# Kernel tuning notes

Hardware: AMD Instinct MI355X
Metric: run time of the kernel (lower is better)

## Reference

```python
import jax, jax.numpy as jnp
import numpy as np

N_BATCH = 1024   # batch size (P=256 identities x K=4 instances)
M_PARTS = 8      # local stripes per image
D_FEAT = 128     # local feature dim
K_PER_ID = 4
MARGIN = 0.3
EPS = 1e-12


def setup_inputs() -> dict:
    key = jax.random.key(0)
    inputs = jax.random.normal(key, (N_BATCH, M_PARTS, D_FEAT), dtype=jnp.float32)
    labels = jnp.arange(N_BATCH, dtype=jnp.int64) // K_PER_ID  # equal samples per class
    return {"inputs": inputs, "labels": labels}


def _shortest_dist(dmat):
    """DTW-style monotone shortest path over the (m, n) grid.
    dmat: [m, n, N, N] -> returns [N, N].
    """
    m = dmat.shape[0]
    # first row: only moves to the right -> cumulative sum over j
    row = jnp.cumsum(dmat[0], axis=0)  # [n, N, N]
    inf = jnp.full(dmat.shape[2:], jnp.inf, dtype=dmat.dtype)

    def step(carry, inp):
        d_ij, up = inp                       # each [N, N]
        val = jnp.minimum(carry, up) + d_ij  # carry=inf at j=0 -> picks `up`
        return val, val

    for i in range(1, m):  # m is a small structural constant (stripes)
        _, row = jax.lax.scan(step, inf, (dmat[i], row))
    return row[-1]  # dist[m-1][n-1], shape [N, N]


def _local_dist(x):
    """x: [N, m, d] (already L2-normalized) -> pairwise aligned dist [N, N]."""
    N, m, d = x.shape
    xf = x.reshape(N * m, d)
    sq = jnp.sum(xf * xf, axis=1)
    dist = sq[:, None] + sq[None, :] - 2.0 * (xf @ xf.T)   # [Nm, Nm]
    dist = jnp.sqrt(jnp.clip(dist, EPS, None))
    dist = jnp.tanh(dist * 0.5)  # (e^d - 1) / (e^d + 1)
    dist = dist.reshape(N, m, N, m).transpose(1, 3, 0, 2)   # [m, n, N, N]
    return _shortest_dist(dist)


def reference(inputs, labels):
    # normalize local features to unit length
    x = inputs / (jnp.linalg.norm(inputs, axis=-1, keepdims=True) + EPS)
    dist_mat = _local_dist(x)  # [N, N]

    # hard example mining
    is_pos = labels[:, None] == labels[None, :]
    dist_ap = jnp.max(jnp.where(is_pos, dist_mat, -jnp.inf), axis=1)
    dist_an = jnp.min(jnp.where(is_pos, jnp.inf, dist_mat), axis=1)

    # MarginRankingLoss(margin)(dist_an, dist_ap, y=1)
    loss = jnp.mean(jnp.maximum(dist_ap - dist_an + MARGIN, 0.0))
    return loss
```

## Files before the change

kernel.cpp:

```cpp
#include <hip/hip_runtime.h>
#include <hip/hip_bf16.h>
#include <math.h>

#define NB 1024
#define MP 8
#define DF 128
#define NV (NB*MP)
#define EPSR 1e-12f
#define MARGIN_ 0.3f

#define GC0  0.4999965f
#define GC1 -0.0416276f
#define GC2  0.0040808f
#define GC3 -0.00035138f
#define GC4  0.00001765f

typedef __bf16    bf16x8 __attribute__((ext_vector_type(8)));
typedef float     f32x4  __attribute__((ext_vector_type(4)));
typedef _Float16  f16x4  __attribute__((ext_vector_type(4)));
typedef _Float16  f16x8  __attribute__((ext_vector_type(8)));

__global__ __launch_bounds__(256) void norm_kernel(const float* __restrict__ x,
                                                   unsigned short* __restrict__ xnb,
                                                   unsigned* __restrict__ ap_max,
                                                   unsigned* __restrict__ an_min) {
    if (blockIdx.x == 0) {
        for (int i = threadIdx.x; i < NB; i += 256) {
            ap_max[i] = 0u;
            an_min[i] = 0x7F800000u;
        }
    }
    const int wave = threadIdx.x >> 6;
    const int lane = threadIdx.x & 63;
    const int v = blockIdx.x * 4 + wave;
    const float e0 = x[v * DF + lane];
    const float e1 = x[v * DF + 64 + lane];
    float s = e0 * e0 + e1 * e1;
    #pragma unroll
    for (int off = 32; off > 0; off >>= 1) s += __shfl_xor(s, off);
    const float inv = 1.0f / (sqrtf(s) + EPSR);
    const __hip_bfloat16 b0 = __float2bfloat16(e0 * inv);
    const __hip_bfloat16 b1 = __float2bfloat16(e1 * inv);
    xnb[v * DF + lane]      = *(const unsigned short*)&b0;
    xnb[v * DF + 64 + lane] = *(const unsigned short*)&b1;
}

__global__ __launch_bounds__(256) void dist_kernel(const unsigned short* __restrict__ xnb,
                                                   const int* __restrict__ labels,
                                                   unsigned* __restrict__ ap_max,
                                                   unsigned* __restrict__ an_min) {
    __shared__ alignas(16) unsigned char smem[32768];
    unsigned short* As = (unsigned short*)smem;
    unsigned short* Bs = (unsigned short*)(smem + 16384);
    unsigned short* E  = (unsigned short*)smem;

    const int idx = (int)blockIdx.x;
    float fsq = sqrtf(8.0f * (float)idx + 1.0f);
    int by = (int)((fsq - 1.0f) * 0.5f);
    while ((by + 1) * (by + 2) / 2 <= idx) ++by;
    while (by * (by + 1) / 2 > idx) --by;
    const int bx = idx - by * (by + 1) / 2;

    const int t    = threadIdx.x;
    const int wave = t >> 6;
    const int lane = t & 63;
    const int wr   = wave >> 1;
    const int wc   = wave & 1;
    const int aBase = bx * 16;
    const int bBase = by * 16;

    const int fr = lane & 15;
    const int fq = lane >> 4;

    f32x4 acc[4][4];
    #pragma unroll
    for (int tr = 0; tr < 4; ++tr)
        #pragma unroll
        for (int tc = 0; tc < 4; ++tc) acc[tr][tc] = (f32x4){0.f, 0.f, 0.f, 0.f};

    #pragma unroll
    for (int kci = 0; kci < 2; ++kci) {
        const int kc = kci * 64;
        if (kci) __syncthreads();
        #pragma unroll
        for (int i = 0; i < 8; ++i) {
            const int ldi  = t + i * 256;
            const int side = ldi >> 10;
            const int r    = (ldi >> 3) & 127;
            const int ch   = ldi & 7;
            const int gv   = (side ? bBase : aBase) * MP + r;
            const uint4 v  = *(const uint4*)&xnb[gv * DF + kc + ch * 8];
            unsigned short* dst = side ? Bs : As;
            *(uint4*)&dst[r * 64 + ((ch ^ (r & 7)) * 8)] = v;
        }
        __syncthreads();

        #pragma unroll
        for (int ksl = 0; ksl < 2; ++ksl) {
            bf16x8 af[4], bfr[4];
            const int ch = ksl * 4 + fq;
            #pragma unroll
            for (int tr = 0; tr < 4; ++tr) {
                const int va = wr * 64 + tr * 16 + fr;
                af[tr] = *(const bf16x8*)&As[va * 64 + ((ch ^ (fr & 7)) * 8)];
            }
            #pragma unroll
            for (int tc = 0; tc < 4; ++tc) {
                const int vb = wc * 64 + tc * 16 + fr;
                bfr[tc] = *(const bf16x8*)&Bs[vb * 64 + ((ch ^ (fr & 7)) * 8)];
            }
            #pragma unroll
            for (int tr = 0; tr < 4; ++tr)
                #pragma unroll
                for (int tc = 0; tc < 4; ++tc)
                    acc[tr][tc] = __builtin_amdgcn_mfma_f32_16x16x32_bf16(
                        af[tr], bfr[tc], acc[tr][tc], 0, 0, 0);
        }
    }
    __syncthreads();

    #pragma unroll
    for (int tr = 0; tr < 4; ++tr) {
        const int r0   = wr * 64 + tr * 16 + fq * 4;
        const int aL   = r0 >> 3;
        const int half = fq & 1;
        #pragma unroll
        for (int tc = 0; tc < 4; ++tc) {
            const int c  = wc * 64 + tc * 16 + fr;
            const int bL = c >> 3, j = c & 7;
            f16x4 hv;
            #pragma unroll
            for (int g = 0; g < 4; ++g) {
                const float d2 = fmaxf(fmaf(-2.0f, acc[tr][tc][g], 2.0f), 0.0f);
                const float d  = __builtin_amdgcn_sqrtf(d2);
                const float pg = fmaf(fmaf(fmaf(fmaf(GC4, d2, GC3), d2, GC2),
                                           d2, GC1), d2, GC0);
                hv[g] = (_Float16)(d * pg);
            }
            const int p   = (aL << 4) + bL;
            const int pos = j ^ (bL & 7);
            *(f16x4*)&E[(p << 6) + (pos << 3) + (half << 2)] = hv;
        }
    }
    __syncthreads();

    f16x8 colv[8];
    {
        const int s = t & 7;
        #pragma unroll
        for (int j = 0; j < 8; ++j)
            colv[j] = *(const f16x8*)&E[(t << 6) + ((j ^ s) << 3)];
    }

    float rowv[8];
    {
        float c = 0.0f;
        #pragma unroll
        for (int j = 0; j < 8; ++j) { c += (float)colv[j][0]; rowv[j] = c; }
    }
    #pragma unroll
    for (int i = 1; i < 8; ++i) {
        float carry = INFINITY;
        #pragma unroll
        for (int j = 0; j < 8; ++j) {
            const float v = fminf(carry, rowv[j]) + (float)colv[j][i];
            rowv[j] = v;
            carry = v;
        }
    }
    const float d = rowv[7];

    const int aG = aBase + (t >> 4);
    const int bG = bBase + (t & 15);
    const bool pos = (labels[aG] == labels[bG]);

    float an_v = pos ? INFINITY : d;
    float ap_v = pos ? d : 0.0f;
    #pragma unroll
    for (int off = 1; off <= 8; off <<= 1) {
        an_v = fminf(an_v, __shfl_xor(an_v, off));
        ap_v = fmaxf(ap_v, __shfl_xor(ap_v, off));
    }
    if ((t & 15) == 0) {
        atomicMin(&an_min[aG], __float_as_uint(an_v));
        if (ap_v > 0.0f) atomicMax(&ap_max[aG], __float_as_uint(ap_v));
    }

    if (bx != by) {
        float an_m = pos ? INFINITY : d;
        float ap_m = pos ? d : 0.0f;
        an_m = fminf(an_m, __shfl_xor(an_m, 16));
        an_m = fminf(an_m, __shfl_xor(an_m, 32));
        ap_m = fmaxf(ap_m, __shfl_xor(ap_m, 16));
        ap_m = fmaxf(ap_m, __shfl_xor(ap_m, 32));
        if (lane < 16) {
            const int bG2 = bBase + lane;
            atomicMin(&an_min[bG2], __float_as_uint(an_m));
            if (ap_m > 0.0f) atomicMax(&ap_max[bG2], __float_as_uint(ap_m));
        }
    }
}

__global__ __launch_bounds__(256) void loss_kernel(const unsigned* __restrict__ ap_max,
                                                   const unsigned* __restrict__ an_min,
                                                   float* __restrict__ out) {
    __shared__ float buf[4];
    const int wave = threadIdx.x >> 6;
    const int lane = threadIdx.x & 63;
    float s = 0.0f;
    for (int i = threadIdx.x; i < NB; i += 256) {
        const float ap = __uint_as_float(ap_max[i]);
        const float an = __uint_as_float(an_min[i]);
        s += fmaxf(ap - an + MARGIN_, 0.0f);
    }
    #pragma unroll
    for (int off = 32; off > 0; off >>= 1) s += __shfl_xor(s, off);
    if (lane == 0) buf[wave] = s;
    __syncthreads();
    if (threadIdx.x == 0) {
        out[0] = (buf[0] + buf[1] + buf[2] + buf[3]) * (1.0f / (float)NB);
    }
}

extern "C" void kernel_launch(void* const* d_in, const int* in_sizes, int n_in,
                              void* d_out, int out_size, void* d_ws, size_t ws_size,
                              hipStream_t stream) {
    const float* x      = (const float*)d_in[0];
    const int*   labels = (const int*)d_in[1];
    float* out = (float*)d_out;

    unsigned short* xnb = (unsigned short*)d_ws;
    unsigned* ap_max = (unsigned*)(xnb + (size_t)NV * DF);
    unsigned* an_min = ap_max + NB;

    const int ntiles = (NB / 16) * (NB / 16 + 1) / 2;

    norm_kernel<<<NV / 4, 256, 0, stream>>>(x, xnb, ap_max, an_min);
    dist_kernel<<<ntiles, 256, 0, stream>>>(xnb, labels, ap_max, an_min);
    loss_kernel<<<1, 256, 0, stream>>>(ap_max, an_min, out);
}
```

Before: 86.71 us.

## Fuse loss reduction into dist kernel via last-block counter, use direct global-to-LDS loads

The separate loss kernel is removed. Each dist block now bumps a global counter after its atomics, and the last block to finish computes the margin loss, which saves one kernel launch. Tile loading switches from register-staged uint4 copies to global_load_lds async copies, with the swizzle moved to the global address side. The fp16 packing uses cvt_pkrtz, which rounds toward zero instead of to nearest. The last-block pattern relies on threadfence ordering, and the direct-to-LDS path depends on compiler support for the builtin.

```diff
diff --git a/kernel.cpp b/kernel.cpp
--- a/kernel.cpp
+++ b/kernel.cpp
@@ -17,18 +17,27 @@
 
 typedef __bf16    bf16x8 __attribute__((ext_vector_type(8)));
 typedef float     f32x4  __attribute__((ext_vector_type(4)));
-typedef _Float16  f16x4  __attribute__((ext_vector_type(4)));
+typedef __fp16    fp16x2 __attribute__((ext_vector_type(2)));
 typedef _Float16  f16x8  __attribute__((ext_vector_type(8)));
+
+__device__ __forceinline__ void async_copy16(const void* g, void* l) {
+    __builtin_amdgcn_global_load_lds(
+        (const __attribute__((address_space(1))) void*)g,
+        (__attribute__((address_space(3))) void*)l,
+        16, 0, 0);
+}
 
 __global__ __launch_bounds__(256) void norm_kernel(const float* __restrict__ x,
                                                    unsigned short* __restrict__ xnb,
                                                    unsigned* __restrict__ ap_max,
-                                                   unsigned* __restrict__ an_min) {
+                                                   unsigned* __restrict__ an_min,
+                                                   unsigned* __restrict__ counter) {
     if (blockIdx.x == 0) {
         for (int i = threadIdx.x; i < NB; i += 256) {
             ap_max[i] = 0u;
             an_min[i] = 0x7F800000u;
         }
+        if (threadIdx.x == 0) *counter = 0u;
     }
     const int wave = threadIdx.x >> 6;
     const int lane = threadIdx.x & 63;
@@ -48,7 +57,9 @@
 __global__ __launch_bounds__(256) void dist_kernel(const unsigned short* __restrict__ xnb,
                                                    const int* __restrict__ labels,
                                                    unsigned* __restrict__ ap_max,
-                                                   unsigned* __restrict__ an_min) {
+                                                   unsigned* __restrict__ an_min,
+                                                   unsigned* __restrict__ counter,
+                                                   float* __restrict__ out) {
     __shared__ alignas(16) unsigned char smem[32768];
     unsigned short* As = (unsigned short*)smem;
     unsigned short* Bs = (unsigned short*)(smem + 16384);
@@ -86,12 +97,14 @@
         for (int i = 0; i < 8; ++i) {
             const int ldi  = t + i * 256;
             const int side = ldi >> 10;
-            const int r    = (ldi >> 3) & 127;
-            const int ch   = ldi & 7;
+            const int slot = ldi & 1023;
+            const int r    = slot >> 3;
+            const int pos  = slot & 7;
+            const int ch   = pos ^ (r & 7);
             const int gv   = (side ? bBase : aBase) * MP + r;
-            const uint4 v  = *(const uint4*)&xnb[gv * DF + kc + ch * 8];
-            unsigned short* dst = side ? Bs : As;
-            *(uint4*)&dst[r * 64 + ((ch ^ (r & 7)) * 8)] = v;
+            const void* g = &xnb[gv * DF + kc + ch * 8];
+            void* l = side ? (void*)&Bs[slot * 8] : (void*)&As[slot * 8];
+            async_copy16(g, l);
         }
         __syncthreads();
 
@@ -128,18 +141,23 @@
         for (int tc = 0; tc < 4; ++tc) {
             const int c  = wc * 64 + tc * 16 + fr;
             const int bL = c >> 3, j = c & 7;
-            f16x4 hv;
+            float td[4];
             #pragma unroll
             for (int g = 0; g < 4; ++g) {
                 const float d2 = fmaxf(fmaf(-2.0f, acc[tr][tc][g], 2.0f), 0.0f);
                 const float d  = __builtin_amdgcn_sqrtf(d2);
                 const float pg = fmaf(fmaf(fmaf(fmaf(GC4, d2, GC3), d2, GC2),
                                            d2, GC1), d2, GC0);
-                hv[g] = (_Float16)(d * pg);
+                td[g] = d * pg;
             }
+            const fp16x2 h01 = __builtin_amdgcn_cvt_pkrtz(td[0], td[1]);
+            const fp16x2 h23 = __builtin_amdgcn_cvt_pkrtz(td[2], td[3]);
+            uint2 w;
+            w.x = __builtin_bit_cast(unsigned, h01);
+            w.y = __builtin_bit_cast(unsigned, h23);
             const int p   = (aL << 4) + bL;
             const int pos = j ^ (bL & 7);
-            *(f16x4*)&E[(p << 6) + (pos << 3) + (half << 2)] = hv;
+            *(uint2*)&E[(p << 6) + (pos << 3) + (half << 2)] = w;
         }
     }
     __syncthreads();
@@ -199,26 +217,29 @@
             if (ap_m > 0.0f) atomicMax(&ap_max[bG2], __float_as_uint(ap_m));
         }
     }
-}
-
-__global__ __launch_bounds__(256) void loss_kernel(const unsigned* __restrict__ ap_max,
-                                                   const unsigned* __restrict__ an_min,
-                                                   float* __restrict__ out) {
-    __shared__ float buf[4];
-    const int wave = threadIdx.x >> 6;
-    const int lane = threadIdx.x & 63;
-    float s = 0.0f;
-    for (int i = threadIdx.x; i < NB; i += 256) {
-        const float ap = __uint_as_float(ap_max[i]);
-        const float an = __uint_as_float(an_min[i]);
-        s += fmaxf(ap - an + MARGIN_, 0.0f);
-    }
-    #pragma unroll
-    for (int off = 32; off > 0; off >>= 1) s += __shfl_xor(s, off);
-    if (lane == 0) buf[wave] = s;
+
+    __threadfence();
+    unsigned* flagp = (unsigned*)smem;
+    if (t == 0) {
+        const unsigned done = atomicAdd(counter, 1u);
+        flagp[0] = (done == (unsigned)(gridDim.x - 1)) ? 1u : 0u;
+    }
     __syncthreads();
-    if (threadIdx.x == 0) {
-        out[0] = (buf[0] + buf[1] + buf[2] + buf[3]) * (1.0f / (float)NB);
+    if (flagp[0] != 0u) {
+        float s = 0.0f;
+        #pragma unroll
+        for (int i = 0; i < NB / 256; ++i) {
+            const int r = i * 256 + t;
+            s += fmaxf(__uint_as_float(ap_max[r]) -
+                       __uint_as_float(an_min[r]) + MARGIN_, 0.0f);
+        }
+        #pragma unroll
+        for (int off = 32; off > 0; off >>= 1) s += __shfl_xor(s, off);
+        float* rbuf = (float*)smem + 16;
+        if (lane == 0) rbuf[wave] = s;
+        __syncthreads();
+        if (t == 0)
+            out[0] = (rbuf[0] + rbuf[1] + rbuf[2] + rbuf[3]) * (1.0f / (float)NB);
     }
 }
 
@@ -230,12 +251,12 @@
     float* out = (float*)d_out;
 
     unsigned short* xnb = (unsigned short*)d_ws;
-    unsigned* ap_max = (unsigned*)(xnb + (size_t)NV * DF);
-    unsigned* an_min = ap_max + NB;
+    unsigned* ap_max  = (unsigned*)(xnb + (size_t)NV * DF);
+    unsigned* an_min  = ap_max + NB;
+    unsigned* counter = an_min + NB;
 
     const int ntiles = (NB / 16) * (NB / 16 + 1) / 2;
 
-    norm_kernel<<<NV / 4, 256, 0, stream>>>(x, xnb, ap_max, an_min);
-    dist_kernel<<<ntiles, 256, 0, stream>>>(xnb, labels, ap_max, an_min);
-    loss_kernel<<<1, 256, 0, stream>>>(ap_max, an_min, out);
-}
+    norm_kernel<<<NV / 4, 256, 0, stream>>>(x, xnb, ap_max, an_min, counter);
+    dist_kernel<<<ntiles, 256, 0, stream>>>(xnb, labels, ap_max, an_min, counter, out);
+}
```

New measurement: 194.6 us. +124.4%, slower.
